# Optimization experiments

Hardware: AMD Instinct MI355X
Metric: run time of the kernel (lower is better)

## Reference

```python
import jax, jax.numpy as jnp
import numpy as np


def entmax15(scores, axis):
    """Exact entmax-1.5 (Peters & Martins 2019), sort-based threshold."""
    s = jnp.moveaxis(scores, axis, -1)
    s = (s - jnp.max(s, axis=-1, keepdims=True)) / 2.0
    d = s.shape[-1]
    srt = jnp.sort(s, axis=-1)[..., ::-1]  # descending
    rho = jnp.arange(1, d + 1, dtype=s.dtype)
    mean = jnp.cumsum(srt, axis=-1) / rho
    mean_sq = jnp.cumsum(srt * srt, axis=-1) / rho
    ss = rho * (mean_sq - mean * mean)
    delta = (1.0 - ss) / rho
    tau = mean - jnp.sqrt(jnp.clip(delta, 0.0, None))
    support = jnp.sum((tau <= srt).astype(jnp.int32), axis=-1)  # support size k*
    tau_star = jnp.take_along_axis(tau, (support - 1)[..., None], axis=-1)
    p = jnp.square(jnp.clip(s - tau_star, 0.0, None))
    return jnp.moveaxis(p, -1, axis)


def setup_inputs() -> dict:
    key = jax.random.key(0)
    k0, k1, k2 = jax.random.split(key, 3)
    B, S, H, A = 64, 2048, 512, 128
    lstm_output = jax.random.normal(k0, (B, S, H), dtype=jnp.float32)
    W1 = jax.random.normal(k1, (H, A), dtype=jnp.float32) * (1.0 / np.sqrt(H))
    b1 = jnp.zeros((A,), dtype=jnp.float32)
    W2 = jax.random.normal(k2, (A, 1), dtype=jnp.float32) * (1.0 / np.sqrt(A))
    b2 = jnp.zeros((1,), dtype=jnp.float32)
    return {"lstm_output": lstm_output, "W1": W1, "b1": b1, "W2": W2, "b2": b2}


def reference(lstm_output, W1, b1, W2, b2):
    # score MLP: Linear -> tanh -> Linear, squeeze(-1)
    h = jnp.tanh(lstm_output @ W1 + b1)            # [B, S, A]
    scores = (h @ W2)[..., 0] + b2[0]              # [B, S]
    weights = entmax15(scores, axis=1)             # sparse weights over seq dim
    context = jnp.einsum('bsh,bs->bh', lstm_output, weights)  # [B, H]
    return (context, weights)
```

## Files before the change

### kernel.cpp

```cpp
#include <hip/hip_runtime.h>
#include <math.h>

#define BB 64
#define SS 2048
#define HH 512
#define AA 128
#define MM (BB*SS)

typedef __attribute__((ext_vector_type(8)))  short short8;
typedef __attribute__((ext_vector_type(16))) float f32x16;

__device__ inline unsigned short f2bf_rne(float f) {
    unsigned u = __float_as_uint(f);
    unsigned r = (u + 0x7fff + ((u >> 16) & 1)) >> 16;
    return (unsigned short)r;
}
__device__ inline float bf2f(unsigned short h) {
    return __uint_as_float(((unsigned)h) << 16);
}
__device__ inline float fast_tanh(float x) {
    float t = __expf(2.0f * x);
    return 1.0f - 2.0f * __builtin_amdgcn_rcpf(t + 1.0f);
}

__global__ __launch_bounds__(256) void prep_w1t(
    const float* __restrict__ W1, unsigned short* __restrict__ W1Th,
    unsigned short* __restrict__ W1Tl)
{
    int idx = blockIdx.x * 256 + threadIdx.x;
    int n = idx & 127, k = idx >> 7;
    float v = W1[k * AA + n];
    unsigned short h = f2bf_rne(v);
    W1Th[n * HH + k] = h;
    W1Tl[n * HH + k] = f2bf_rne(v - bf2f(h));
}

__global__ __launch_bounds__(256, 2) void score_mfma(
    const float* __restrict__ X,
    const unsigned short* __restrict__ W1Th,
    const unsigned short* __restrict__ W1Tl,
    const float* __restrict__ b1, const float* __restrict__ W2,
    const float* __restrict__ b2, float* __restrict__ scores)
{
    __shared__ unsigned short B_lds[2][2][4][AA][8];

    const int tid  = threadIdx.x;
    const int wave = tid >> 6;
    const int lane = tid & 63;
    const int l31  = lane & 31;
    const int half = lane >> 5;
    const int m0   = blockIdx.x * 256;

    int sb_hilo[4], sb_g[4], sb_n[4];
    #pragma unroll
    for (int i = 0; i < 4; i++) {
        int c = tid + 256 * i;
        sb_hilo[i] = c >> 9;
        sb_g[i]    = (c >> 7) & 3;
        sb_n[i]    = c & 127;
    }

    const float* aptr0 = X + (size_t)(m0 + wave * 64      + l31) * HH + half * 8;
    const float* aptr1 = X + (size_t)(m0 + wave * 64 + 32 + l31) * HH + half * 8;

    f32x16 acc[2][4];
    #pragma unroll
    for (int mt = 0; mt < 2; mt++)
        #pragma unroll
        for (int nt = 0; nt < 4; nt++)
            #pragma unroll
            for (int j = 0; j < 16; j++) acc[mt][nt][j] = 0.f;

    short8 breg[4];
    float4 apre[2][2][2];

    #pragma unroll
    for (int i = 0; i < 4; i++) {
        const unsigned short* src = sb_hilo[i] ? W1Tl : W1Th;
        breg[i] = *(const short8*)(src + (size_t)sb_n[i] * HH + sb_g[i] * 8);
    }
    #pragma unroll
    for (int s = 0; s < 2; s++) {
        apre[0][s][0] = *(const float4*)(aptr0 + s * 16);
        apre[0][s][1] = *(const float4*)(aptr0 + s * 16 + 4);
        apre[1][s][0] = *(const float4*)(aptr1 + s * 16);
        apre[1][s][1] = *(const float4*)(aptr1 + s * 16 + 4);
    }
    #pragma unroll
    for (int i = 0; i < 4; i++)
        *(short8*)&B_lds[0][sb_hilo[i]][sb_g[i]][sb_n[i]][0] = breg[i];
    __syncthreads();

    for (int it = 0; it < 16; it++) {
        const int cur = it & 1;

        if (it < 15) {
            #pragma unroll
            for (int i = 0; i < 4; i++) {
                const unsigned short* src = sb_hilo[i] ? W1Tl : W1Th;
                breg[i] = *(const short8*)(src + (size_t)sb_n[i] * HH
                                           + (it + 1) * 32 + sb_g[i] * 8);
            }
        }

        short8 ah[2][2], al[2][2];
        #pragma unroll
        for (int mt = 0; mt < 2; mt++)
            #pragma unroll
            for (int s = 0; s < 2; s++) {
                float fs[8];
                *(float4*)&fs[0] = apre[mt][s][0];
                *(float4*)&fs[4] = apre[mt][s][1];
                #pragma unroll
                for (int j = 0; j < 8; j++) {
                    unsigned short h = f2bf_rne(fs[j]);
                    ah[mt][s][j] = (short)h;
                    float r = fs[j] - bf2f(h);
                    al[mt][s][j] = (short)(__float_as_uint(r) >> 16);
                }
            }

        if (it < 15) {
            #pragma unroll
            for (int s = 0; s < 2; s++) {
                apre[0][s][0] = *(const float4*)(aptr0 + (it + 1) * 32 + s * 16);
                apre[0][s][1] = *(const float4*)(aptr0 + (it + 1) * 32 + s * 16 + 4);
                apre[1][s][0] = *(const float4*)(aptr1 + (it + 1) * 32 + s * 16);
                apre[1][s][1] = *(const float4*)(aptr1 + (it + 1) * 32 + s * 16 + 4);
            }
        }

        #pragma unroll
        for (int s = 0; s < 2; s++) {
            const int gr = s * 2 + half;
            #pragma unroll
            for (int nt = 0; nt < 4; nt++) {
                short8 bh = *(const short8*)&B_lds[cur][0][gr][nt * 32 + l31][0];
                short8 bl = *(const short8*)&B_lds[cur][1][gr][nt * 32 + l31][0];
                acc[0][nt] = __builtin_amdgcn_mfma_f32_32x32x16_bf16(ah[0][s], bh, acc[0][nt], 0, 0, 0);
                acc[0][nt] = __builtin_amdgcn_mfma_f32_32x32x16_bf16(ah[0][s], bl, acc[0][nt], 0, 0, 0);
                acc[0][nt] = __builtin_amdgcn_mfma_f32_32x32x16_bf16(al[0][s], bh, acc[0][nt], 0, 0, 0);
                acc[1][nt] = __builtin_amdgcn_mfma_f32_32x32x16_bf16(ah[1][s], bh, acc[1][nt], 0, 0, 0);
                acc[1][nt] = __builtin_amdgcn_mfma_f32_32x32x16_bf16(ah[1][s], bl, acc[1][nt], 0, 0, 0);
                acc[1][nt] = __builtin_amdgcn_mfma_f32_32x32x16_bf16(al[1][s], bh, acc[1][nt], 0, 0, 0);
            }
        }

        if (it < 15) {
            #pragma unroll
            for (int i = 0; i < 4; i++)
                *(short8*)&B_lds[cur ^ 1][sb_hilo[i]][sb_g[i]][sb_n[i]][0] = breg[i];
        }
        __syncthreads();
    }

    const float bb2 = b2[0];
    #pragma unroll
    for (int mt = 0; mt < 2; mt++) {
        float part[16];
        #pragma unroll
        for (int r = 0; r < 16; r++) part[r] = 0.f;
        #pragma unroll
        for (int nt = 0; nt < 4; nt++) {
            int n = nt * 32 + l31;
            float bias = b1[n];
            float w2   = W2[n];
            #pragma unroll
            for (int r = 0; r < 16; r++)
                part[r] += fast_tanh(acc[mt][nt][r] + bias) * w2;
        }
        #pragma unroll
        for (int off = 16; off > 0; off >>= 1)
            #pragma unroll
            for (int r = 0; r < 16; r++)
                part[r] += __shfl_xor(part[r], off);
        if (l31 == 0) {
            #pragma unroll
            for (int r = 0; r < 16; r++) {
                int row = (r & 3) + 8 * (r >> 2) + 4 * half;
                scores[m0 + wave * 64 + mt * 32 + row] = part[r] + bb2;
            }
        }
    }
}

__global__ __launch_bounds__(256) void entmax_bisect(
    const float* __restrict__ scores, float* __restrict__ weights)
{
    __shared__ float red[4];
    const int t = threadIdx.x, b = blockIdx.x;
    const int wv = t >> 6, ln = t & 63;
    const float* row = scores + (size_t)b * SS;

    float v[8];
    #pragma unroll
    for (int i = 0; i < 8; i++) v[i] = row[t + 256 * i];

    float mx = v[0];
    #pragma unroll
    for (int i = 1; i < 8; i++) mx = fmaxf(mx, v[i]);
    #pragma unroll
    for (int off = 32; off > 0; off >>= 1) mx = fmaxf(mx, __shfl_xor(mx, off));
    if (ln == 0) red[wv] = mx;
    __syncthreads();
    mx = fmaxf(fmaxf(red[0], red[1]), fmaxf(red[2], red[3]));

    #pragma unroll
    for (int i = 0; i < 8; i++) v[i] = (v[i] - mx) * 0.5f;

    float lo = -1.0f, hi = 0.0f;
    for (int it = 0; it < 32; it++) {
        float tm = 0.5f * (lo + hi);
        float s = 0.f;
        #pragma unroll
        for (int i = 0; i < 8; i++) {
            float d = fmaxf(v[i] - tm, 0.f);
            s = fmaf(d, d, s);
        }
        #pragma unroll
        for (int off = 32; off > 0; off >>= 1) s += __shfl_xor(s, off);
        __syncthreads();
        if (ln == 0) red[wv] = s;
        __syncthreads();
        s = red[0] + red[1] + red[2] + red[3];
        if (s >= 1.0f) lo = tm; else hi = tm;
    }
    float tau = 0.5f * (lo + hi);

    #pragma unroll
    for (int i = 0; i < 8; i++) {
        float d = fmaxf(v[i] - tau, 0.f);
        weights[(size_t)b * SS + t + 256 * i] = d * d;
    }
}

__global__ __launch_bounds__(256) void context_kernel(
    const float* __restrict__ X, const float* __restrict__ weights,
    float* __restrict__ ctx)
{
    const int b = blockIdx.y;
    const int chunk = blockIdx.x;
    const int tid = threadIdx.x;
    const float* wrow  = weights + (size_t)b * SS + chunk * 64;
    const float* xbase = X + ((size_t)b * SS + (size_t)chunk * 64) * HH;
    float acc0 = 0.f, acc1 = 0.f;
    bool any = false;
    for (int s = 0; s < 64; s++) {
        float w = wrow[s];
        if (w != 0.f) {
            any = true;
            float2 x = *(const float2*)(xbase + (size_t)s * HH + 2 * tid);
            acc0 = fmaf(x.x, w, acc0);
            acc1 = fmaf(x.y, w, acc1);
        }
    }
    if (any) {
        atomicAdd(&ctx[b * HH + 2 * tid],     acc0);
        atomicAdd(&ctx[b * HH + 2 * tid + 1], acc1);
    }
}

extern "C" void kernel_launch(void* const* d_in, const int* in_sizes, int n_in,
                              void* d_out, int out_size, void* d_ws, size_t ws_size,
                              hipStream_t stream) {
    const float* X  = (const float*)d_in[0];
    const float* W1 = (const float*)d_in[1];
    const float* b1 = (const float*)d_in[2];
    const float* W2 = (const float*)d_in[3];
    const float* b2 = (const float*)d_in[4];

    float* out     = (float*)d_out;
    float* ctx     = out;
    float* weights = out + BB * HH;
    float* scores  = weights;

    unsigned short* W1Th = (unsigned short*)d_ws;
    unsigned short* W1Tl = W1Th + (size_t)AA * HH;

    hipMemsetAsync(ctx, 0, (size_t)BB * HH * sizeof(float), stream);
    prep_w1t<<<dim3(256), 256, 0, stream>>>(W1, W1Th, W1Tl);
    score_mfma<<<dim3(MM / 256), 256, 0, stream>>>(X, W1Th, W1Tl, b1, W2, b2, scores);
    entmax_bisect<<<dim3(BB), 256, 0, stream>>>(scores, weights);
    context_kernel<<<dim3(32, BB), 256, 0, stream>>>(X, weights, ctx);
}
```

Measured before the change: 403.2 us.

## Prelayout W1 as MFMA fragments, drop LDS staging, split N across waves

New measurement: 416.4 us. 1.03x slower.

```diff
diff --git a/kernel.cpp b/kernel.cpp
--- a/kernel.cpp
+++ b/kernel.cpp
@@ -6,6 +6,7 @@
 #define HH 512
 #define AA 128
 #define MM (BB*SS)
+#define BM 128
 
 typedef __attribute__((ext_vector_type(8)))  short short8;
 typedef __attribute__((ext_vector_type(16))) float f32x16;
@@ -23,86 +24,63 @@
     return 1.0f - 2.0f * __builtin_amdgcn_rcpf(t + 1.0f);
 }
 
-__global__ __launch_bounds__(256) void prep_w1t(
-    const float* __restrict__ W1, unsigned short* __restrict__ W1Th,
-    unsigned short* __restrict__ W1Tl)
+__global__ __launch_bounds__(256) void prep_w1frag(
+    const float* __restrict__ W1, unsigned short* __restrict__ Bf)
 {
     int idx = blockIdx.x * 256 + threadIdx.x;
-    int n = idx & 127, k = idx >> 7;
+    int n = idx >> 9, k = idx & 511;
     float v = W1[k * AA + n];
-    unsigned short h = f2bf_rne(v);
-    W1Th[n * HH + k] = h;
-    W1Tl[n * HH + k] = f2bf_rne(v - bf2f(h));
-}
-
-__global__ __launch_bounds__(256, 2) void score_mfma(
-    const float* __restrict__ X,
-    const unsigned short* __restrict__ W1Th,
-    const unsigned short* __restrict__ W1Tl,
+    unsigned short h  = f2bf_rne(v);
+    unsigned short lo = (unsigned short)(__float_as_uint(v - bf2f(h)) >> 16);
+    int it = k >> 5, kk = k & 31;
+    int s  = kk >> 4, hf = (kk >> 3) & 1, j = kk & 7;
+    int nt = n >> 5, lane = hf * 32 + (n & 31);
+    size_t base = ((((size_t)(it * 2 + s) * 2 + 0) * 4 + nt) * 64 + lane) * 8 + j;
+    size_t off  = (size_t)4 * 64 * 8;
+    Bf[base]       = h;
+    Bf[base + off] = lo;
+}
+
+__global__ __launch_bounds__(256) void score_mfma(
+    const float* __restrict__ X, const unsigned short* __restrict__ Bf,
     const float* __restrict__ b1, const float* __restrict__ W2,
     const float* __restrict__ b2, float* __restrict__ scores)
 {
-    __shared__ unsigned short B_lds[2][2][4][AA][8];
+    __shared__ float part[2][2][32][2];
 
     const int tid  = threadIdx.x;
     const int wave = tid >> 6;
     const int lane = tid & 63;
     const int l31  = lane & 31;
     const int half = lane >> 5;
-    const int m0   = blockIdx.x * 256;
-
-    int sb_hilo[4], sb_g[4], sb_n[4];
-    #pragma unroll
-    for (int i = 0; i < 4; i++) {
-        int c = tid + 256 * i;
-        sb_hilo[i] = c >> 9;
-        sb_g[i]    = (c >> 7) & 3;
-        sb_n[i]    = c & 127;
-    }
-
-    const float* aptr0 = X + (size_t)(m0 + wave * 64      + l31) * HH + half * 8;
-    const float* aptr1 = X + (size_t)(m0 + wave * 64 + 32 + l31) * HH + half * 8;
-
-    f32x16 acc[2][4];
+    const int wm   = wave >> 1;
+    const int wn   = wave & 1;
+    const int m0   = blockIdx.x * BM;
+
+    const float* arow[2];
     #pragma unroll
     for (int mt = 0; mt < 2; mt++)
-        #pragma unroll
-        for (int nt = 0; nt < 4; nt++)
-            #pragma unroll
-            for (int j = 0; j < 16; j++) acc[mt][nt][j] = 0.f;
-
-    short8 breg[4];
+        arow[mt] = X + (size_t)(m0 + wm * 64 + mt * 32 + l31) * HH;
+
+    f32x16 acc[2][2];
+    #pragma unroll
+    for (int mt = 0; mt < 2; mt++)
+        #pragma unroll
+        for (int nt = 0; nt < 2; nt++)
+            #pragma unroll
+            for (int r = 0; r < 16; r++) acc[mt][nt][r] = 0.f;
+
     float4 apre[2][2][2];
-
-    #pragma unroll
-    for (int i = 0; i < 4; i++) {
-        const unsigned short* src = sb_hilo[i] ? W1Tl : W1Th;
-        breg[i] = *(const short8*)(src + (size_t)sb_n[i] * HH + sb_g[i] * 8);
-    }
-    #pragma unroll
-    for (int s = 0; s < 2; s++) {
-        apre[0][s][0] = *(const float4*)(aptr0 + s * 16);
-        apre[0][s][1] = *(const float4*)(aptr0 + s * 16 + 4);
-        apre[1][s][0] = *(const float4*)(aptr1 + s * 16);
-        apre[1][s][1] = *(const float4*)(aptr1 + s * 16 + 4);
-    }
-    #pragma unroll
-    for (int i = 0; i < 4; i++)
-        *(short8*)&B_lds[0][sb_hilo[i]][sb_g[i]][sb_n[i]][0] = breg[i];
-    __syncthreads();
+    #pragma unroll
+    for (int mt = 0; mt < 2; mt++)
+        #pragma unroll
+        for (int s = 0; s < 2; s++) {
+            const float* p = arow[mt] + s * 16 + half * 8;
+            apre[mt][s][0] = *(const float4*)p;
+            apre[mt][s][1] = *(const float4*)(p + 4);
+        }
 
     for (int it = 0; it < 16; it++) {
-        const int cur = it & 1;
-
-        if (it < 15) {
-            #pragma unroll
-            for (int i = 0; i < 4; i++) {
-                const unsigned short* src = sb_hilo[i] ? W1Tl : W1Th;
-                breg[i] = *(const short8*)(src + (size_t)sb_n[i] * HH
-                                           + (it + 1) * 32 + sb_g[i] * 8);
-            }
-        }
-
         short8 ah[2][2], al[2][2];
         #pragma unroll
         for (int mt = 0; mt < 2; mt++)
@@ -115,72 +93,70 @@
                 for (int j = 0; j < 8; j++) {
                     unsigned short h = f2bf_rne(fs[j]);
                     ah[mt][s][j] = (short)h;
-                    float r = fs[j] - bf2f(h);
-                    al[mt][s][j] = (short)(__float_as_uint(r) >> 16);
+                    al[mt][s][j] = (short)(__float_as_uint(fs[j] - bf2f(h)) >> 16);
                 }
             }
-
         if (it < 15) {
             #pragma unroll
-            for (int s = 0; s < 2; s++) {
-                apre[0][s][0] = *(const float4*)(aptr0 + (it + 1) * 32 + s * 16);
-                apre[0][s][1] = *(const float4*)(aptr0 + (it + 1) * 32 + s * 16 + 4);
-                apre[1][s][0] = *(const float4*)(aptr1 + (it + 1) * 32 + s * 16);
-                apre[1][s][1] = *(const float4*)(aptr1 + (it + 1) * 32 + s * 16 + 4);
+            for (int mt = 0; mt < 2; mt++)
+                #pragma unroll
+                for (int s = 0; s < 2; s++) {
+                    const float* p = arow[mt] + (it + 1) * 32 + s * 16 + half * 8;
+                    apre[mt][s][0] = *(const float4*)p;
+                    apre[mt][s][1] = *(const float4*)(p + 4);
+                }
+        }
+        #pragma unroll
+        for (int s = 0; s < 2; s++) {
+            const unsigned short* bsrc =
+                Bf + ((size_t)(it * 2 + s) * 2) * (4 * 64 * 8) + (size_t)lane * 8;
+            #pragma unroll
+            for (int nt = 0; nt < 2; nt++) {
+                const int ntg = wn * 2 + nt;
+                short8 bh = *(const short8*)(bsrc + (size_t)ntg * (64 * 8));
+                short8 bl = *(const short8*)(bsrc + (size_t)(4 + ntg) * (64 * 8));
+                #pragma unroll
+                for (int mt = 0; mt < 2; mt++) {
+                    acc[mt][nt] = __builtin_amdgcn_mfma_f32_32x32x16_bf16(ah[mt][s], bh, acc[mt][nt], 0, 0, 0);
+                    acc[mt][nt] = __builtin_amdgcn_mfma_f32_32x32x16_bf16(ah[mt][s], bl, acc[mt][nt], 0, 0, 0);
+                    acc[mt][nt] = __builtin_amdgcn_mfma_f32_32x32x16_bf16(al[mt][s], bh, acc[mt][nt], 0, 0, 0);
+                }
             }
         }
-
-        #pragma unroll
-        for (int s = 0; s < 2; s++) {
-            const int gr = s * 2 + half;
-            #pragma unroll
-            for (int nt = 0; nt < 4; nt++) {
-                short8 bh = *(const short8*)&B_lds[cur][0][gr][nt * 32 + l31][0];
-                short8 bl = *(const short8*)&B_lds[cur][1][gr][nt * 32 + l31][0];
-                acc[0][nt] = __builtin_amdgcn_mfma_f32_32x32x16_bf16(ah[0][s], bh, acc[0][nt], 0, 0, 0);
-                acc[0][nt] = __builtin_amdgcn_mfma_f32_32x32x16_bf16(ah[0][s], bl, acc[0][nt], 0, 0, 0);
-                acc[0][nt] = __builtin_amdgcn_mfma_f32_32x32x16_bf16(al[0][s], bh, acc[0][nt], 0, 0, 0);
-                acc[1][nt] = __builtin_amdgcn_mfma_f32_32x32x16_bf16(ah[1][s], bh, acc[1][nt], 0, 0, 0);
-                acc[1][nt] = __builtin_amdgcn_mfma_f32_32x32x16_bf16(ah[1][s], bl, acc[1][nt], 0, 0, 0);
-                acc[1][nt] = __builtin_amdgcn_mfma_f32_32x32x16_bf16(al[1][s], bh, acc[1][nt], 0, 0, 0);
-            }
-        }
-
-        if (it < 15) {
-            #pragma unroll
-            for (int i = 0; i < 4; i++)
-                *(short8*)&B_lds[cur ^ 1][sb_hilo[i]][sb_g[i]][sb_n[i]][0] = breg[i];
-        }
-        __syncthreads();
-    }
-
-    const float bb2 = b2[0];
+    }
+
     #pragma unroll
     for (int mt = 0; mt < 2; mt++) {
-        float part[16];
-        #pragma unroll
-        for (int r = 0; r < 16; r++) part[r] = 0.f;
-        #pragma unroll
-        for (int nt = 0; nt < 4; nt++) {
-            int n = nt * 32 + l31;
+        float p[16];
+        #pragma unroll
+        for (int r = 0; r < 16; r++) p[r] = 0.f;
+        #pragma unroll
+        for (int nt = 0; nt < 2; nt++) {
+            int n = wn * 64 + nt * 32 + l31;
             float bias = b1[n];
             float w2   = W2[n];
             #pragma unroll
             for (int r = 0; r < 16; r++)
-                part[r] += fast_tanh(acc[mt][nt][r] + bias) * w2;
+                p[r] += fast_tanh(acc[mt][nt][r] + bias) * w2;
         }
         #pragma unroll
         for (int off = 16; off > 0; off >>= 1)
             #pragma unroll
             for (int r = 0; r < 16; r++)
-                part[r] += __shfl_xor(part[r], off);
+                p[r] += __shfl_xor(p[r], off);
         if (l31 == 0) {
             #pragma unroll
             for (int r = 0; r < 16; r++) {
                 int row = (r & 3) + 8 * (r >> 2) + 4 * half;
-                scores[m0 + wave * 64 + mt * 32 + row] = part[r] + bb2;
+                part[wm][mt][row][wn] = p[r];
             }
         }
+    }
+    __syncthreads();
+    if (tid < 128) {
+        int wmm = tid >> 6, mtt = (tid >> 5) & 1, row = tid & 31;
+        scores[m0 + wmm * 64 + mtt * 32 + row] =
+            part[wmm][mtt][row][0] + part[wmm][mtt][row][1] + b2[0];
     }
 }
 
@@ -274,12 +250,11 @@
     float* weights = out + BB * HH;
     float* scores  = weights;
 
-    unsigned short* W1Th = (unsigned short*)d_ws;
-    unsigned short* W1Tl = W1Th + (size_t)AA * HH;
+    unsigned short* Bf = (unsigned short*)d_ws;
 
     hipMemsetAsync(ctx, 0, (size_t)BB * HH * sizeof(float), stream);
-    prep_w1t<<<dim3(256), 256, 0, stream>>>(W1, W1Th, W1Tl);
-    score_mfma<<<dim3(MM / 256), 256, 0, stream>>>(X, W1Th, W1Tl, b1, W2, b2, scores);
+    prep_w1frag<<<dim3(256), 256, 0, stream>>>(W1, Bf);
+    score_mfma<<<dim3(MM / BM), 256, 0, stream>>>(X, Bf, b1, W2, b2, scores);
     entmax_bisect<<<dim3(BB), 256, 0, stream>>>(scores, weights);
     context_kernel<<<dim3(32, BB), 256, 0, stream>>>(X, weights, ctx);
 }
```
